# Kernel optimization log

Hardware: AMD Instinct MI355X
Metric: run time of the kernel (lower is better)

Reference implementation:

```python
import jax, jax.numpy as jnp
import numpy as np

N_NODES = 100000
N_EDGES = 1000000
KEY_DIM = 128
VAL_DIM = 64


def setup_inputs() -> dict:
    key = jax.random.key(0)
    k0, k1, k2, k3, k4, k5 = jax.random.split(key, 6)
    triples = jax.random.randint(k0, (N_EDGES, 3), 0, N_NODES, dtype=jnp.int64)
    ent_feats = jax.random.normal(k1, (N_NODES, KEY_DIM), dtype=jnp.float32)
    att_feats = jax.random.normal(k2, (N_NODES, KEY_DIM), dtype=jnp.float32)
    val_feats = jax.random.normal(k3, (N_NODES, VAL_DIM), dtype=jnp.float32)
    # a: Linear(2*key_dim, 1) -> weight vector [2k], bias [1]
    a_w = jax.random.normal(k4, (2 * KEY_DIM,), dtype=jnp.float32) * (1.0 / np.sqrt(2 * KEY_DIM))
    a_b = jnp.zeros((1,), dtype=jnp.float32)
    W = jax.random.normal(k5, (KEY_DIM + VAL_DIM, KEY_DIM), dtype=jnp.float32) * (1.0 / np.sqrt(KEY_DIM + VAL_DIM))
    return {"attribute_triples": triples, "ent_feats": ent_feats,
            "att_feats": att_feats, "val_feats": val_feats,
            "a_w": a_w, "a_b": a_b, "W": W}


def reference(attribute_triples, ent_feats, att_feats, val_feats, a_w, a_b, W):
    N = ent_feats.shape[0]
    h = attribute_triples[:, 0]
    att = attribute_triples[:, 1]
    val = attribute_triples[:, 2]
    # edge attention score: a([e_h ; a_att]) -> leaky_relu -> exp
    e_h = ent_feats[h]            # [E, K]
    a_f = att_feats[att]          # [E, K]
    score = jnp.concatenate((e_h, a_f), axis=-1) @ a_w + a_b[0]   # [E]
    score = jnp.exp(jax.nn.leaky_relu(score, negative_slope=0.2))
    # segment softmax denominator per head node
    row_sum = jax.ops.segment_sum(score, h, num_segments=N)       # [N]
    attention_p = score / row_sum[h]                               # [E]
    # projected edge messages, weighted by attention, scattered to nodes
    av = jnp.concatenate((a_f, val_feats[val]), axis=-1) @ W       # [E, K]
    av = av * attention_p[:, None]
    to_feats = jax.ops.segment_sum(av, h, num_segments=N)          # [N, K]
    return jax.nn.elu(to_feats + ent_feats)
```

## Files before the change

kernel.cpp:

```cpp
#include <hip/hip_runtime.h>

#define N_NODES 100000
#define N_EDGES 1000000
#define CAP     40

typedef __attribute__((ext_vector_type(8))) short short8;
typedef __attribute__((ext_vector_type(4))) short short4v;
typedef __attribute__((ext_vector_type(4))) float float4_t;
typedef __attribute__((ext_vector_type(2))) float floatx2;
typedef unsigned long long ull;

__device__ __forceinline__ unsigned short f_to_bf(float f) {
    union { float f; unsigned int i; } c; c.f = f;
    unsigned int x = c.i;
    unsigned int r = x + 0x7fffu + ((x >> 16) & 1u);
    return (unsigned short)(r >> 16);
}
__device__ __forceinline__ float bf_to_f(unsigned short u) {
    union { unsigned int i; float f; } c; c.i = ((unsigned int)u) << 16; return c.f;
}
__device__ __forceinline__ unsigned int pack2(float x, float y) {
    return (unsigned int)f_to_bf(x) | ((unsigned int)f_to_bf(y) << 16);
}
__device__ __forceinline__ unsigned short f_to_h(float f) {
    union { float f; unsigned int i; } c; c.f = f;
    unsigned int i = c.i;
    unsigned int e = ((i >> 23) & 0xffu) - 112u;
    unsigned int m = i & 0x7fffffu;
    unsigned int r = (e << 10) | (m >> 13);
    r += (m >> 12) & 1u;
    return (unsigned short)r;
}
__device__ __forceinline__ float h_to_f(unsigned short h) {
    union { unsigned int i; float f; } c;
    c.i = (((unsigned int)(h & 0x7fffu)) << 13) + 0x38000000u;
    return c.f;
}
__device__ __forceinline__ floatx2 up2(unsigned int u) {
    union { unsigned int i; float f; } lo, hi;
    lo.i = u << 16; hi.i = u & 0xffff0000u;
    floatx2 r; r.x = lo.f; r.y = hi.f; return r;
}
__device__ __forceinline__ int clampi(int x) {
    return x < 0 ? 0 : (x >= N_NODES ? N_NODES - 1 : x);
}

__global__ __launch_bounds__(256)
void k_node_scores(const float* __restrict__ ent,
                   const float* __restrict__ attf,
                   const float* __restrict__ valf,
                   const float* __restrict__ aw,
                   float* __restrict__ s_ent, float* __restrict__ s_att,
                   unsigned short* __restrict__ attb,
                   unsigned short* __restrict__ valb) {
    int node = (int)((blockIdx.x * blockDim.x + threadIdx.x) >> 6);
    int lane = threadIdx.x & 63;
    if (node >= N_NODES) return;
    const float2* aw2 = (const float2*)aw;
    float2 we = aw2[lane];
    float2 wa = aw2[64 + lane];
    float2 e2 = ((const float2*)ent)[(size_t)node * 64 + lane];
    float2 a2 = ((const float2*)attf)[(size_t)node * 64 + lane];
    if (attb) ((unsigned int*)attb)[(size_t)node * 64 + lane] = pack2(a2.x, a2.y);
    if (valb) valb[(size_t)node * 64 + lane] = f_to_bf(valf[(size_t)node * 64 + lane]);
    float se = e2.x * we.x + e2.y * we.y;
    float sa = a2.x * wa.x + a2.y * wa.y;
#pragma unroll
    for (int off = 32; off >= 1; off >>= 1) {
        se += __shfl_xor(se, off, 64);
        sa += __shfl_xor(sa, off, 64);
    }
    if (lane == 0) { s_ent[node] = se; s_att[node] = sa; }
}

__global__ __launch_bounds__(256)
void k_prepW(const float* __restrict__ W, unsigned short* __restrict__ Wt) {
    int i = (int)(blockIdx.x * blockDim.x + threadIdx.x);
    if (i >= 192 * 128) return;
    int c = i / 192, k = i - c * 192;
    Wt[i] = f_to_bf(W[k * 128 + c]);
}

__global__ __launch_bounds__(256)
void k_place(const int* __restrict__ tri,
             const float* __restrict__ s_ent, const float* __restrict__ s_att,
             const float* __restrict__ abp,
             int* __restrict__ cursor, ull* __restrict__ edges) {
    int e = (int)(blockIdx.x * blockDim.x + threadIdx.x);
    if (e >= N_EDGES) return;
    int h = clampi(tri[3 * e]);
    int a = clampi(tri[3 * e + 1]);
    int v = clampi(tri[3 * e + 2]);
    float s = s_ent[h] + s_att[a] + abp[0];
    s = s > 0.f ? s : 0.2f * s;
    float sc = __expf(s);
    int slot = atomicAdd(&cursor[h], 1);
    if (slot < CAP) {
        ull pk = (ull)(unsigned)a | ((ull)(unsigned)v << 17) | ((ull)f_to_h(sc) << 34);
        edges[(size_t)h * CAP + slot] = pk;
    }
}

__global__ __launch_bounds__(256)
void k_fused_bf(const int* __restrict__ cursor, const ull* __restrict__ edges,
                const unsigned short* __restrict__ attb, const unsigned short* __restrict__ valb,
                const unsigned short* __restrict__ Wt, const float* __restrict__ ent,
                float* __restrict__ out) {
    __shared__ unsigned short Gl[16][200];
    int w = threadIdx.x >> 6, lane = threadIdx.x & 63;
    int grp = lane >> 4, l = lane & 15;
    int base = (int)blockIdx.x * 16;
    int nb = base + w * 4;

    int4 cnt4 = *(const int4*)(cursor + nb);
    int li = lane < CAP ? lane : CAP - 1;
    ull edr[4];
#pragma unroll
    for (int nn = 0; nn < 4; ++nn) edr[nn] = edges[(size_t)(nb + nn) * CAP + li];

    const char* ab = (const char*)attb;
    const char* vb = (const char*)valb;

#pragma unroll
    for (int nn = 0; nn < 4; ++nn) {
        int cnt = (nn == 0) ? cnt4.x : (nn == 1) ? cnt4.y : (nn == 2) ? cnt4.z : cnt4.w;
        cnt = cnt > CAP ? CAP : cnt;
        ull edreg = edr[nn];
        floatx2 aa0 = {0.f, 0.f}, aa1 = {0.f, 0.f}, aa2 = {0.f, 0.f}, aa3 = {0.f, 0.f};
        floatx2 av0 = {0.f, 0.f}, av1 = {0.f, 0.f};
        float rsum = 0.f;
        int kmax = (cnt + 7) >> 3;
        for (int k = 0; k < kmax; ++k) {
            int j0 = grp + (k << 3), j1 = j0 + 4;
            bool m0 = j0 < cnt, m1 = j1 < cnt;
            ull e0 = __shfl(edreg, m0 ? j0 : 0, 64);
            ull e1 = __shfl(edreg, m1 ? j1 : 0, 64);
            unsigned a0 = m0 ? (unsigned)(e0 & 0x1FFFFu) : (unsigned)N_NODES;
            unsigned v0 = m0 ? (unsigned)((e0 >> 17) & 0x1FFFFu) : (unsigned)N_NODES;
            float   sc0 = m0 ? h_to_f((unsigned short)(e0 >> 34)) : 0.f;
            unsigned a1 = m1 ? (unsigned)(e1 & 0x1FFFFu) : (unsigned)N_NODES;
            unsigned v1 = m1 ? (unsigned)((e1 >> 17) & 0x1FFFFu) : (unsigned)N_NODES;
            float   sc1 = m1 ? h_to_f((unsigned short)(e1 >> 34)) : 0.f;
            uint4 A0 = *(const uint4*)(ab + (a0 << 8) + (l << 4));
            uint2 V0 = *(const uint2*)(vb + (v0 << 7) + (l << 3));
            uint4 A1 = *(const uint4*)(ab + (a1 << 8) + (l << 4));
            uint2 V1 = *(const uint2*)(vb + (v1 << 7) + (l << 3));
            rsum += sc0 + sc1;
            floatx2 s0; s0.x = sc0; s0.y = sc0;
            floatx2 s1; s1.x = sc1; s1.y = sc1;
            aa0 += s0 * up2(A0.x); aa1 += s0 * up2(A0.y);
            aa2 += s0 * up2(A0.z); aa3 += s0 * up2(A0.w);
            av0 += s0 * up2(V0.x); av1 += s0 * up2(V0.y);
            aa0 += s1 * up2(A1.x); aa1 += s1 * up2(A1.y);
            aa2 += s1 * up2(A1.z); aa3 += s1 * up2(A1.w);
            av0 += s1 * up2(V1.x); av1 += s1 * up2(V1.y);
        }
#define RED2(x) x += __shfl_xor(x, 16, 64); x += __shfl_xor(x, 32, 64)
        RED2(aa0.x); RED2(aa0.y); RED2(aa1.x); RED2(aa1.y);
        RED2(aa2.x); RED2(aa2.y); RED2(aa3.x); RED2(aa3.y);
        RED2(av0.x); RED2(av0.y); RED2(av1.x); RED2(av1.y);
        RED2(rsum);
#undef RED2
        if (grp == 0) {
            float inv = rsum > 0.f ? 1.f / rsum : 0.f;
            unsigned short* gp = &Gl[w * 4 + nn][0];
            uint4 pk;
            pk.x = pack2(aa0.x * inv, aa0.y * inv);
            pk.y = pack2(aa1.x * inv, aa1.y * inv);
            pk.z = pack2(aa2.x * inv, aa2.y * inv);
            pk.w = pack2(aa3.x * inv, aa3.y * inv);
            *(uint4*)(gp + l * 8) = pk;
            uint2 pv; pv.x = pack2(av0.x * inv, av0.y * inv);
            pv.y = pack2(av1.x * inv, av1.y * inv);
            *(uint2*)(gp + 128 + l * 4) = pv;
        }
    }
    __syncthreads();

    int quad = grp, mn = l;
    float4_t acc0 = {0.f, 0.f, 0.f, 0.f}, acc1 = {0.f, 0.f, 0.f, 0.f};
#pragma unroll
    for (int kt = 0; kt < 6; ++kt) {
        short8 afr = *(const short8*)(&Gl[mn][quad * 8 + kt * 32]);
        short8 b0 = *(const short8*)(Wt + (size_t)((w * 2 + 0) * 16 + mn) * 192 + quad * 8 + kt * 32);
        short8 b1 = *(const short8*)(Wt + (size_t)((w * 2 + 1) * 16 + mn) * 192 + quad * 8 + kt * 32);
        acc0 = __builtin_amdgcn_mfma_f32_16x16x32_bf16(afr, b0, acc0, 0, 0, 0);
        acc1 = __builtin_amdgcn_mfma_f32_16x16x32_bf16(afr, b1, acc1, 0, 0, 0);
    }
#pragma unroll
    for (int cti = 0; cti < 2; ++cti) {
        float4_t acc = cti ? acc1 : acc0;
        int col = (w * 2 + cti) * 16 + mn;
#pragma unroll
        for (int r = 0; r < 4; ++r) {
            int node = base + quad * 4 + r;
            float x = acc[r] + ent[(size_t)node * 128 + col];
            out[(size_t)node * 128 + col] = x > 0.f ? x : expm1f(x);
        }
    }
}

template<int ABF, int VBF>
__global__ __launch_bounds__(256)
void k_fused(const int* __restrict__ cursor, const ull* __restrict__ edges,
             const float* __restrict__ attf, const float* __restrict__ valf,
             const unsigned short* __restrict__ attb, const unsigned short* __restrict__ valb,
             const unsigned short* __restrict__ Wt, const float* __restrict__ ent,
             float* __restrict__ out) {
    __shared__ unsigned short Gl[16][200];
    int w = threadIdx.x >> 6, lane = threadIdx.x & 63;
    int grp = lane >> 4, l = lane & 15;
    int base = (int)blockIdx.x * 16;

    for (int nn = 0; nn < 4; ++nn) {
        int node = base + w * 4 + nn;
        int cnt = cursor[node]; if (cnt > CAP) cnt = CAP;
        size_t beg = (size_t)node * CAP;
        float aa[8] = {0.f, 0.f, 0.f, 0.f, 0.f, 0.f, 0.f, 0.f};
        float av[4] = {0.f, 0.f, 0.f, 0.f};
        float rsum = 0.f;
        for (int j = grp; j < cnt; j += 4) {
            ull ed = edges[beg + j];
            int a = (int)(ed & 0x1FFFFu);
            int v = (int)((ed >> 17) & 0x1FFFFu);
            float sc = h_to_f((unsigned short)(ed >> 34));
            rsum += sc;
            if (ABF) {
                short8 af = *(const short8*)(attb + (size_t)a * 128 + l * 8);
#pragma unroll
                for (int q = 0; q < 8; ++q) aa[q] += sc * bf_to_f((unsigned short)af[q]);
            } else {
                const float4_t* ap = (const float4_t*)(attf + (size_t)a * 128);
                float4_t f0 = ap[l], f1 = ap[16 + l];
#pragma unroll
                for (int q = 0; q < 4; ++q) { aa[q] += sc * f0[q]; aa[4 + q] += sc * f1[q]; }
            }
            if (VBF) {
                short4v vf = *(const short4v*)(valb + (size_t)v * 64 + l * 4);
#pragma unroll
                for (int q = 0; q < 4; ++q) av[q] += sc * bf_to_f((unsigned short)vf[q]);
            } else {
                float4_t fv = ((const float4_t*)(valf + (size_t)v * 64))[l];
#pragma unroll
                for (int q = 0; q < 4; ++q) av[q] += sc * fv[q];
            }
        }
#pragma unroll
        for (int q = 0; q < 8; ++q) {
            aa[q] += __shfl_xor(aa[q], 16, 64);
            aa[q] += __shfl_xor(aa[q], 32, 64);
        }
#pragma unroll
        for (int q = 0; q < 4; ++q) {
            av[q] += __shfl_xor(av[q], 16, 64);
            av[q] += __shfl_xor(av[q], 32, 64);
        }
        rsum += __shfl_xor(rsum, 16, 64);
        rsum += __shfl_xor(rsum, 32, 64);
        if (grp == 0) {
            float inv = rsum > 0.f ? 1.f / rsum : 0.f;
            unsigned short* gp = &Gl[w * 4 + nn][0];
            if (ABF) {
                uint4 pk;
                pk.x = pack2(aa[0] * inv, aa[1] * inv);
                pk.y = pack2(aa[2] * inv, aa[3] * inv);
                pk.z = pack2(aa[4] * inv, aa[5] * inv);
                pk.w = pack2(aa[6] * inv, aa[7] * inv);
                *(uint4*)(gp + l * 8) = pk;
            } else {
                uint2 p0; p0.x = pack2(aa[0] * inv, aa[1] * inv); p0.y = pack2(aa[2] * inv, aa[3] * inv);
                *(uint2*)(gp + l * 4) = p0;
                uint2 p1; p1.x = pack2(aa[4] * inv, aa[5] * inv); p1.y = pack2(aa[6] * inv, aa[7] * inv);
                *(uint2*)(gp + 64 + l * 4) = p1;
            }
            uint2 pv; pv.x = pack2(av[0] * inv, av[1] * inv); pv.y = pack2(av[2] * inv, av[3] * inv);
            *(uint2*)(gp + 128 + l * 4) = pv;
        }
    }
    __syncthreads();

    int quad = grp, mn = l;
    float4_t acc0 = {0.f, 0.f, 0.f, 0.f}, acc1 = {0.f, 0.f, 0.f, 0.f};
#pragma unroll
    for (int kt = 0; kt < 6; ++kt) {
        short8 afr = *(const short8*)(&Gl[mn][quad * 8 + kt * 32]);
        short8 b0 = *(const short8*)(Wt + (size_t)((w * 2 + 0) * 16 + mn) * 192 + quad * 8 + kt * 32);
        short8 b1 = *(const short8*)(Wt + (size_t)((w * 2 + 1) * 16 + mn) * 192 + quad * 8 + kt * 32);
        acc0 = __builtin_amdgcn_mfma_f32_16x16x32_bf16(afr, b0, acc0, 0, 0, 0);
        acc1 = __builtin_amdgcn_mfma_f32_16x16x32_bf16(afr, b1, acc1, 0, 0, 0);
    }
#pragma unroll
    for (int cti = 0; cti < 2; ++cti) {
        float4_t acc = cti ? acc1 : acc0;
        int col = (w * 2 + cti) * 16 + mn;
#pragma unroll
        for (int r = 0; r < 4; ++r) {
            int node = base + quad * 4 + r;
            float x = acc[r] + ent[(size_t)node * 128 + col];
            out[(size_t)node * 128 + col] = x > 0.f ? x : expm1f(x);
        }
    }
}

extern "C" void kernel_launch(void* const* d_in, const int* in_sizes, int n_in,
                              void* d_out, int out_size, void* d_ws, size_t ws_size,
                              hipStream_t stream) {
    const int*   tri  = (const int*)d_in[0];
    const float* ent  = (const float*)d_in[1];
    const float* attf = (const float*)d_in[2];
    const float* valf = (const float*)d_in[3];
    const float* aw   = (const float*)d_in[4];
    const float* ab   = (const float*)d_in[5];
    const float* W    = (const float*)d_in[6];
    float* out = (float*)d_out;

    char* ws = (char*)d_ws;
    size_t off = 0;
    int*   cursor = (int*)(ws + off);   off += (size_t)N_NODES * 4;
    float* s_ent  = (float*)(ws + off); off += (size_t)N_NODES * 4;
    float* s_att  = (float*)(ws + off); off += (size_t)N_NODES * 4;
    unsigned short* Wt = (unsigned short*)(ws + off); off += 192 * 128 * 2;
    ull* edges = (ull*)(ws + off);      off += (size_t)N_NODES * CAP * 8;
    unsigned short* attb = (unsigned short*)(ws + off);
    off += (size_t)(N_NODES + 1) * 128 * 2;
    size_t need_a = off;
    unsigned short* valb = (unsigned short*)(ws + off);
    off += (size_t)(N_NODES + 1) * 64 * 2;
    size_t need_av = off;
    int abf = ws_size >= need_a;
    int vbf = ws_size >= need_av;

    hipMemsetAsync(cursor, 0, (size_t)N_NODES * 4, stream);
    if (abf) hipMemsetAsync(attb + (size_t)N_NODES * 128, 0, 256, stream);
    if (vbf) hipMemsetAsync(valb + (size_t)N_NODES * 64, 0, 128, stream);

    k_node_scores<<<N_NODES / 4, 256, 0, stream>>>(ent, attf, valf, aw, s_ent, s_att,
                                                   abf ? attb : (unsigned short*)nullptr,
                                                   vbf ? valb : (unsigned short*)nullptr);
    k_prepW<<<(192 * 128 + 255) / 256, 256, 0, stream>>>(W, Wt);
    k_place<<<(N_EDGES + 255) / 256, 256, 0, stream>>>(tri, s_ent, s_att, ab, cursor, edges);
    if (abf && vbf)
        k_fused_bf<<<N_NODES / 16, 256, 0, stream>>>(cursor, edges, attb, valb, Wt, ent, out);
    else if (abf)
        k_fused<1, 0><<<N_NODES / 16, 256, 0, stream>>>(cursor, edges, attf, valf, attb, valb, Wt, ent, out);
    else
        k_fused<0, 0><<<N_NODES / 16, 256, 0, stream>>>(cursor, edges, attf, valf, attb, valb, Wt, ent, out);
}
```

Before: 332.0 us.

## Switch gathered features and weights to fp16 with packed half accumulation

Converts the attribute/value feature tables and W from bf16 to fp16, and accumulates the per-edge weighted sums with packed fp16 vector math (including the cross-lane reductions) instead of fp32. The MFMA switches to the f16 variant. Nontemporal loads and stores are added on triples, the edge list, ent and out, and masked edges now gather row 0 instead of a zeroed sentinel row. The aim is to halve accumulation ALU and register cost and to reduce cache pollution, at the risk of fp16 overflow or precision loss when summing up to 40 scaled features.

```diff
diff --git a/kernel.cpp b/kernel.cpp
--- a/kernel.cpp
+++ b/kernel.cpp
@@ -4,24 +4,14 @@
 #define N_EDGES 1000000
 #define CAP     40
 
-typedef __attribute__((ext_vector_type(8))) short short8;
-typedef __attribute__((ext_vector_type(4))) short short4v;
 typedef __attribute__((ext_vector_type(4))) float float4_t;
-typedef __attribute__((ext_vector_type(2))) float floatx2;
+typedef __attribute__((ext_vector_type(2))) _Float16 half2v;
+typedef __attribute__((ext_vector_type(4))) _Float16 half4v;
+typedef __attribute__((ext_vector_type(8))) _Float16 half8v;
+typedef __attribute__((ext_vector_type(2))) unsigned int uint2v;
+typedef __attribute__((ext_vector_type(4))) unsigned int uint4v;
 typedef unsigned long long ull;
 
-__device__ __forceinline__ unsigned short f_to_bf(float f) {
-    union { float f; unsigned int i; } c; c.f = f;
-    unsigned int x = c.i;
-    unsigned int r = x + 0x7fffu + ((x >> 16) & 1u);
-    return (unsigned short)(r >> 16);
-}
-__device__ __forceinline__ float bf_to_f(unsigned short u) {
-    union { unsigned int i; float f; } c; c.i = ((unsigned int)u) << 16; return c.f;
-}
-__device__ __forceinline__ unsigned int pack2(float x, float y) {
-    return (unsigned int)f_to_bf(x) | ((unsigned int)f_to_bf(y) << 16);
-}
 __device__ __forceinline__ unsigned short f_to_h(float f) {
     union { float f; unsigned int i; } c; c.f = f;
     unsigned int i = c.i;
@@ -36,10 +26,15 @@
     c.i = (((unsigned int)(h & 0x7fffu)) << 13) + 0x38000000u;
     return c.f;
 }
-__device__ __forceinline__ floatx2 up2(unsigned int u) {
-    union { unsigned int i; float f; } lo, hi;
-    lo.i = u << 16; hi.i = u & 0xffff0000u;
-    floatx2 r; r.x = lo.f; r.y = hi.f; return r;
+__device__ __forceinline__ unsigned int packh2(float x, float y) {
+    half2v h; h.x = (_Float16)x; h.y = (_Float16)y;
+    return __builtin_bit_cast(unsigned int, h);
+}
+__device__ __forceinline__ unsigned int h2add(unsigned int a, unsigned int b) {
+    half2v x = __builtin_bit_cast(half2v, a);
+    half2v y = __builtin_bit_cast(half2v, b);
+    half2v r = x + y;
+    return __builtin_bit_cast(unsigned int, r);
 }
 __device__ __forceinline__ int clampi(int x) {
     return x < 0 ? 0 : (x >= N_NODES ? N_NODES - 1 : x);
@@ -61,8 +56,11 @@
     float2 wa = aw2[64 + lane];
     float2 e2 = ((const float2*)ent)[(size_t)node * 64 + lane];
     float2 a2 = ((const float2*)attf)[(size_t)node * 64 + lane];
-    if (attb) ((unsigned int*)attb)[(size_t)node * 64 + lane] = pack2(a2.x, a2.y);
-    if (valb) valb[(size_t)node * 64 + lane] = f_to_bf(valf[(size_t)node * 64 + lane]);
+    if (attb) ((unsigned int*)attb)[(size_t)node * 64 + lane] = packh2(a2.x, a2.y);
+    if (valb) {
+        float vv = valf[(size_t)node * 64 + lane];
+        valb[(size_t)node * 64 + lane] = __builtin_bit_cast(unsigned short, (_Float16)vv);
+    }
     float se = e2.x * we.x + e2.y * we.y;
     float sa = a2.x * wa.x + a2.y * wa.y;
 #pragma unroll
@@ -78,7 +76,7 @@
     int i = (int)(blockIdx.x * blockDim.x + threadIdx.x);
     if (i >= 192 * 128) return;
     int c = i / 192, k = i - c * 192;
-    Wt[i] = f_to_bf(W[k * 128 + c]);
+    Wt[i] = __builtin_bit_cast(unsigned short, (_Float16)W[k * 128 + c]);
 }
 
 __global__ __launch_bounds__(256)
@@ -88,24 +86,24 @@
              int* __restrict__ cursor, ull* __restrict__ edges) {
     int e = (int)(blockIdx.x * blockDim.x + threadIdx.x);
     if (e >= N_EDGES) return;
-    int h = clampi(tri[3 * e]);
-    int a = clampi(tri[3 * e + 1]);
-    int v = clampi(tri[3 * e + 2]);
+    int h = clampi(__builtin_nontemporal_load(tri + 3 * e));
+    int a = clampi(__builtin_nontemporal_load(tri + 3 * e + 1));
+    int v = clampi(__builtin_nontemporal_load(tri + 3 * e + 2));
     float s = s_ent[h] + s_att[a] + abp[0];
     s = s > 0.f ? s : 0.2f * s;
     float sc = __expf(s);
     int slot = atomicAdd(&cursor[h], 1);
     if (slot < CAP) {
         ull pk = (ull)(unsigned)a | ((ull)(unsigned)v << 17) | ((ull)f_to_h(sc) << 34);
-        edges[(size_t)h * CAP + slot] = pk;
-    }
-}
-
-__global__ __launch_bounds__(256)
-void k_fused_bf(const int* __restrict__ cursor, const ull* __restrict__ edges,
-                const unsigned short* __restrict__ attb, const unsigned short* __restrict__ valb,
-                const unsigned short* __restrict__ Wt, const float* __restrict__ ent,
-                float* __restrict__ out) {
+        __builtin_nontemporal_store(pk, edges + (size_t)h * CAP + slot);
+    }
+}
+
+__global__ __launch_bounds__(256)
+void k_fused_h(const int* __restrict__ cursor, const ull* __restrict__ edges,
+               const unsigned short* __restrict__ attb, const unsigned short* __restrict__ valb,
+               const unsigned short* __restrict__ Wt, const float* __restrict__ ent,
+               float* __restrict__ out) {
     __shared__ unsigned short Gl[16][200];
     int w = threadIdx.x >> 6, lane = threadIdx.x & 63;
     int grp = lane >> 4, l = lane & 15;
@@ -113,21 +111,23 @@
     int nb = base + w * 4;
 
     int4 cnt4 = *(const int4*)(cursor + nb);
-    int li = lane < CAP ? lane : CAP - 1;
+    int cns[4] = {cnt4.x, cnt4.y, cnt4.z, cnt4.w};
     ull edr[4];
 #pragma unroll
-    for (int nn = 0; nn < 4; ++nn) edr[nn] = edges[(size_t)(nb + nn) * CAP + li];
-
-    const char* ab = (const char*)attb;
-    const char* vb = (const char*)valb;
-
-#pragma unroll
     for (int nn = 0; nn < 4; ++nn) {
-        int cnt = (nn == 0) ? cnt4.x : (nn == 1) ? cnt4.y : (nn == 2) ? cnt4.z : cnt4.w;
-        cnt = cnt > CAP ? CAP : cnt;
+        int c = cns[nn]; c = c > CAP ? CAP : c; cns[nn] = c;
+        int li = lane < c ? lane : 0;
+        edr[nn] = __builtin_nontemporal_load(edges + (size_t)(nb + nn) * CAP + li);
+    }
+    const half8v* ap = (const half8v*)attb;
+    const half4v* vp = (const half4v*)valb;
+
+#pragma unroll
+    for (int nn = 0; nn < 4; ++nn) {
+        int cnt = cns[nn];
         ull edreg = edr[nn];
-        floatx2 aa0 = {0.f, 0.f}, aa1 = {0.f, 0.f}, aa2 = {0.f, 0.f}, aa3 = {0.f, 0.f};
-        floatx2 av0 = {0.f, 0.f}, av1 = {0.f, 0.f};
+        half8v accA = {};
+        half4v accV = {};
         float rsum = 0.f;
         int kmax = (cnt + 7) >> 3;
         for (int k = 0; k < kmax; ++k) {
@@ -135,44 +135,46 @@
             bool m0 = j0 < cnt, m1 = j1 < cnt;
             ull e0 = __shfl(edreg, m0 ? j0 : 0, 64);
             ull e1 = __shfl(edreg, m1 ? j1 : 0, 64);
-            unsigned a0 = m0 ? (unsigned)(e0 & 0x1FFFFu) : (unsigned)N_NODES;
-            unsigned v0 = m0 ? (unsigned)((e0 >> 17) & 0x1FFFFu) : (unsigned)N_NODES;
-            float   sc0 = m0 ? h_to_f((unsigned short)(e0 >> 34)) : 0.f;
-            unsigned a1 = m1 ? (unsigned)(e1 & 0x1FFFFu) : (unsigned)N_NODES;
-            unsigned v1 = m1 ? (unsigned)((e1 >> 17) & 0x1FFFFu) : (unsigned)N_NODES;
-            float   sc1 = m1 ? h_to_f((unsigned short)(e1 >> 34)) : 0.f;
-            uint4 A0 = *(const uint4*)(ab + (a0 << 8) + (l << 4));
-            uint2 V0 = *(const uint2*)(vb + (v0 << 7) + (l << 3));
-            uint4 A1 = *(const uint4*)(ab + (a1 << 8) + (l << 4));
-            uint2 V1 = *(const uint2*)(vb + (v1 << 7) + (l << 3));
-            rsum += sc0 + sc1;
-            floatx2 s0; s0.x = sc0; s0.y = sc0;
-            floatx2 s1; s1.x = sc1; s1.y = sc1;
-            aa0 += s0 * up2(A0.x); aa1 += s0 * up2(A0.y);
-            aa2 += s0 * up2(A0.z); aa3 += s0 * up2(A0.w);
-            av0 += s0 * up2(V0.x); av1 += s0 * up2(V0.y);
-            aa0 += s1 * up2(A1.x); aa1 += s1 * up2(A1.y);
-            aa2 += s1 * up2(A1.z); aa3 += s1 * up2(A1.w);
-            av0 += s1 * up2(V1.x); av1 += s1 * up2(V1.y);
-        }
-#define RED2(x) x += __shfl_xor(x, 16, 64); x += __shfl_xor(x, 32, 64)
-        RED2(aa0.x); RED2(aa0.y); RED2(aa1.x); RED2(aa1.y);
-        RED2(aa2.x); RED2(aa2.y); RED2(aa3.x); RED2(aa3.y);
-        RED2(av0.x); RED2(av0.y); RED2(av1.x); RED2(av1.y);
-        RED2(rsum);
-#undef RED2
+            int a0 = (int)(e0 & 0x1FFFFu), v0 = (int)((e0 >> 17) & 0x1FFFFu);
+            int a1 = (int)(e1 & 0x1FFFFu), v1 = (int)((e1 >> 17) & 0x1FFFFu);
+            _Float16 s0 = m0 ? __builtin_bit_cast(_Float16, (unsigned short)(e0 >> 34)) : (_Float16)0.f;
+            _Float16 s1 = m1 ? __builtin_bit_cast(_Float16, (unsigned short)(e1 >> 34)) : (_Float16)0.f;
+            half8v A0 = ap[a0 * 16 + l];
+            half4v V0 = vp[v0 * 16 + l];
+            half8v A1 = ap[a1 * 16 + l];
+            half4v V1 = vp[v1 * 16 + l];
+            rsum += (float)s0 + (float)s1;
+            accA += A0 * s0;
+            accV += V0 * s0;
+            accA += A1 * s1;
+            accV += V1 * s1;
+        }
+        uint4v ua = __builtin_bit_cast(uint4v, accA);
+        uint2v uv = __builtin_bit_cast(uint2v, accV);
+#pragma unroll
+        for (int q = 0; q < 4; ++q) {
+            unsigned int x = ua[q];
+            x = h2add(x, __shfl_xor(x, 16, 64));
+            x = h2add(x, __shfl_xor(x, 32, 64));
+            ua[q] = x;
+        }
+#pragma unroll
+        for (int q = 0; q < 2; ++q) {
+            unsigned int x = uv[q];
+            x = h2add(x, __shfl_xor(x, 16, 64));
+            x = h2add(x, __shfl_xor(x, 32, 64));
+            uv[q] = x;
+        }
+        rsum += __shfl_xor(rsum, 16, 64);
+        rsum += __shfl_xor(rsum, 32, 64);
         if (grp == 0) {
             float inv = rsum > 0.f ? 1.f / rsum : 0.f;
+            _Float16 ih = (_Float16)inv;
+            half8v gA = __builtin_bit_cast(half8v, ua) * ih;
+            half4v gV = __builtin_bit_cast(half4v, uv) * ih;
             unsigned short* gp = &Gl[w * 4 + nn][0];
-            uint4 pk;
-            pk.x = pack2(aa0.x * inv, aa0.y * inv);
-            pk.y = pack2(aa1.x * inv, aa1.y * inv);
-            pk.z = pack2(aa2.x * inv, aa2.y * inv);
-            pk.w = pack2(aa3.x * inv, aa3.y * inv);
-            *(uint4*)(gp + l * 8) = pk;
-            uint2 pv; pv.x = pack2(av0.x * inv, av0.y * inv);
-            pv.y = pack2(av1.x * inv, av1.y * inv);
-            *(uint2*)(gp + 128 + l * 4) = pv;
+            *(half8v*)(gp + l * 8) = gA;
+            *(half4v*)(gp + 128 + l * 4) = gV;
         }
     }
     __syncthreads();
@@ -181,11 +183,11 @@
     float4_t acc0 = {0.f, 0.f, 0.f, 0.f}, acc1 = {0.f, 0.f, 0.f, 0.f};
 #pragma unroll
     for (int kt = 0; kt < 6; ++kt) {
-        short8 afr = *(const short8*)(&Gl[mn][quad * 8 + kt * 32]);
-        short8 b0 = *(const short8*)(Wt + (size_t)((w * 2 + 0) * 16 + mn) * 192 + quad * 8 + kt * 32);
-        short8 b1 = *(const short8*)(Wt + (size_t)((w * 2 + 1) * 16 + mn) * 192 + quad * 8 + kt * 32);
-        acc0 = __builtin_amdgcn_mfma_f32_16x16x32_bf16(afr, b0, acc0, 0, 0, 0);
-        acc1 = __builtin_amdgcn_mfma_f32_16x16x32_bf16(afr, b1, acc1, 0, 0, 0);
+        half8v afr = *(const half8v*)(&Gl[mn][quad * 8 + kt * 32]);
+        half8v b0 = *(const half8v*)(Wt + (size_t)((w * 2 + 0) * 16 + mn) * 192 + quad * 8 + kt * 32);
+        half8v b1 = *(const half8v*)(Wt + (size_t)((w * 2 + 1) * 16 + mn) * 192 + quad * 8 + kt * 32);
+        acc0 = __builtin_amdgcn_mfma_f32_16x16x32_f16(afr, b0, acc0, 0, 0, 0);
+        acc1 = __builtin_amdgcn_mfma_f32_16x16x32_f16(afr, b1, acc1, 0, 0, 0);
     }
 #pragma unroll
     for (int cti = 0; cti < 2; ++cti) {
@@ -194,19 +196,18 @@
 #pragma unroll
         for (int r = 0; r < 4; ++r) {
             int node = base + quad * 4 + r;
-            float x = acc[r] + ent[(size_t)node * 128 + col];
-            out[(size_t)node * 128 + col] = x > 0.f ? x : expm1f(x);
-        }
-    }
-}
-
-template<int ABF, int VBF>
-__global__ __launch_bounds__(256)
-void k_fused(const int* __restrict__ cursor, const ull* __restrict__ edges,
-             const float* __restrict__ attf, const float* __restrict__ valf,
-             const unsigned short* __restrict__ attb, const unsigned short* __restrict__ valb,
-             const unsigned short* __restrict__ Wt, const float* __restrict__ ent,
-             float* __restrict__ out) {
+            float x = acc[r] + __builtin_nontemporal_load(ent + (size_t)node * 128 + col);
+            __builtin_nontemporal_store(x > 0.f ? x : expm1f(x),
+                                        out + (size_t)node * 128 + col);
+        }
+    }
+}
+
+__global__ __launch_bounds__(256)
+void k_fused_f32(const int* __restrict__ cursor, const ull* __restrict__ edges,
+                 const float* __restrict__ attf, const float* __restrict__ valf,
+                 const unsigned short* __restrict__ Wt, const float* __restrict__ ent,
+                 float* __restrict__ out) {
     __shared__ unsigned short Gl[16][200];
     int w = threadIdx.x >> 6, lane = threadIdx.x & 63;
     int grp = lane >> 4, l = lane & 15;
@@ -225,24 +226,12 @@
             int v = (int)((ed >> 17) & 0x1FFFFu);
             float sc = h_to_f((unsigned short)(ed >> 34));
             rsum += sc;
-            if (ABF) {
-                short8 af = *(const short8*)(attb + (size_t)a * 128 + l * 8);
-#pragma unroll
-                for (int q = 0; q < 8; ++q) aa[q] += sc * bf_to_f((unsigned short)af[q]);
-            } else {
-                const float4_t* ap = (const float4_t*)(attf + (size_t)a * 128);
-                float4_t f0 = ap[l], f1 = ap[16 + l];
-#pragma unroll
-                for (int q = 0; q < 4; ++q) { aa[q] += sc * f0[q]; aa[4 + q] += sc * f1[q]; }
-            }
-            if (VBF) {
-                short4v vf = *(const short4v*)(valb + (size_t)v * 64 + l * 4);
-#pragma unroll
-                for (int q = 0; q < 4; ++q) av[q] += sc * bf_to_f((unsigned short)vf[q]);
-            } else {
-                float4_t fv = ((const float4_t*)(valf + (size_t)v * 64))[l];
-#pragma unroll
-                for (int q = 0; q < 4; ++q) av[q] += sc * fv[q];
+            const float4_t* ap = (const float4_t*)(attf + (size_t)a * 128);
+            float4_t f0 = ap[l], f1 = ap[16 + l];
+            float4_t fv = ((const float4_t*)(valf + (size_t)v * 64))[l];
+#pragma unroll
+            for (int q = 0; q < 4; ++q) {
+                aa[q] += sc * f0[q]; aa[4 + q] += sc * f1[q]; av[q] += sc * fv[q];
             }
         }
 #pragma unroll
@@ -260,20 +249,11 @@
         if (grp == 0) {
             float inv = rsum > 0.f ? 1.f / rsum : 0.f;
             unsigned short* gp = &Gl[w * 4 + nn][0];
-            if (ABF) {
-                uint4 pk;
-                pk.x = pack2(aa[0] * inv, aa[1] * inv);
-                pk.y = pack2(aa[2] * inv, aa[3] * inv);
-                pk.z = pack2(aa[4] * inv, aa[5] * inv);
-                pk.w = pack2(aa[6] * inv, aa[7] * inv);
-                *(uint4*)(gp + l * 8) = pk;
-            } else {
-                uint2 p0; p0.x = pack2(aa[0] * inv, aa[1] * inv); p0.y = pack2(aa[2] * inv, aa[3] * inv);
-                *(uint2*)(gp + l * 4) = p0;
-                uint2 p1; p1.x = pack2(aa[4] * inv, aa[5] * inv); p1.y = pack2(aa[6] * inv, aa[7] * inv);
-                *(uint2*)(gp + 64 + l * 4) = p1;
-            }
-            uint2 pv; pv.x = pack2(av[0] * inv, av[1] * inv); pv.y = pack2(av[2] * inv, av[3] * inv);
+            uint2 p0; p0.x = packh2(aa[0] * inv, aa[1] * inv); p0.y = packh2(aa[2] * inv, aa[3] * inv);
+            *(uint2*)(gp + l * 4) = p0;
+            uint2 p1; p1.x = packh2(aa[4] * inv, aa[5] * inv); p1.y = packh2(aa[6] * inv, aa[7] * inv);
+            *(uint2*)(gp + 64 + l * 4) = p1;
+            uint2 pv; pv.x = packh2(av[0] * inv, av[1] * inv); pv.y = packh2(av[2] * inv, av[3] * inv);
             *(uint2*)(gp + 128 + l * 4) = pv;
         }
     }
@@ -283,11 +263,11 @@
     float4_t acc0 = {0.f, 0.f, 0.f, 0.f}, acc1 = {0.f, 0.f, 0.f, 0.f};
 #pragma unroll
     for (int kt = 0; kt < 6; ++kt) {
-        short8 afr = *(const short8*)(&Gl[mn][quad * 8 + kt * 32]);
-        short8 b0 = *(const short8*)(Wt + (size_t)((w * 2 + 0) * 16 + mn) * 192 + quad * 8 + kt * 32);
-        short8 b1 = *(const short8*)(Wt + (size_t)((w * 2 + 1) * 16 + mn) * 192 + quad * 8 + kt * 32);
-        acc0 = __builtin_amdgcn_mfma_f32_16x16x32_bf16(afr, b0, acc0, 0, 0, 0);
-        acc1 = __builtin_amdgcn_mfma_f32_16x16x32_bf16(afr, b1, acc1, 0, 0, 0);
+        half8v afr = *(const half8v*)(&Gl[mn][quad * 8 + kt * 32]);
+        half8v b0 = *(const half8v*)(Wt + (size_t)((w * 2 + 0) * 16 + mn) * 192 + quad * 8 + kt * 32);
+        half8v b1 = *(const half8v*)(Wt + (size_t)((w * 2 + 1) * 16 + mn) * 192 + quad * 8 + kt * 32);
+        acc0 = __builtin_amdgcn_mfma_f32_16x16x32_f16(afr, b0, acc0, 0, 0, 0);
+        acc1 = __builtin_amdgcn_mfma_f32_16x16x32_f16(afr, b1, acc1, 0, 0, 0);
     }
 #pragma unroll
     for (int cti = 0; cti < 2; ++cti) {
@@ -321,28 +301,20 @@
     float* s_att  = (float*)(ws + off); off += (size_t)N_NODES * 4;
     unsigned short* Wt = (unsigned short*)(ws + off); off += 192 * 128 * 2;
     ull* edges = (ull*)(ws + off);      off += (size_t)N_NODES * CAP * 8;
-    unsigned short* attb = (unsigned short*)(ws + off);
-    off += (size_t)(N_NODES + 1) * 128 * 2;
-    size_t need_a = off;
-    unsigned short* valb = (unsigned short*)(ws + off);
-    off += (size_t)(N_NODES + 1) * 64 * 2;
-    size_t need_av = off;
-    int abf = ws_size >= need_a;
-    int vbf = ws_size >= need_av;
+    unsigned short* attb = (unsigned short*)(ws + off); off += (size_t)N_NODES * 128 * 2;
+    unsigned short* valb = (unsigned short*)(ws + off); off += (size_t)N_NODES * 64 * 2;
+    size_t need = off;
+    int h16 = ws_size >= need;
 
     hipMemsetAsync(cursor, 0, (size_t)N_NODES * 4, stream);
-    if (abf) hipMemsetAsync(attb + (size_t)N_NODES * 128, 0, 256, stream);
-    if (vbf) hipMemsetAsync(valb + (size_t)N_NODES * 64, 0, 128, stream);
 
     k_node_scores<<<N_NODES / 4, 256, 0, stream>>>(ent, attf, valf, aw, s_ent, s_att,
-                                                   abf ? attb : (unsigned short*)nullptr,
-                                                   vbf ? valb : (unsigned short*)nullptr);
+                                                   h16 ? attb : (unsigned short*)nullptr,
+                                                   h16 ? valb : (unsigned short*)nullptr);
     k_prepW<<<(192 * 128 + 255) / 256, 256, 0, stream>>>(W, Wt);
     k_place<<<(N_EDGES + 255) / 256, 256, 0, stream>>>(tri, s_ent, s_att, ab, cursor, edges);
-    if (abf && vbf)
-        k_fused_bf<<<N_NODES / 16, 256, 0, stream>>>(cursor, edges, attb, valb, Wt, ent, out);
-    else if (abf)
-        k_fused<1, 0><<<N_NODES / 16, 256, 0, stream>>>(cursor, edges, attf, valf, attb, valb, Wt, ent, out);
+    if (h16)
+        k_fused_h<<<N_NODES / 16, 256, 0, stream>>>(cursor, edges, attb, valb, Wt, ent, out);
     else
-        k_fused<0, 0><<<N_NODES / 16, 256, 0, stream>>>(cursor, edges, attf, valf, attb, valb, Wt, ent, out);
-}
+        k_fused_f32<<<N_NODES / 16, 256, 0, stream>>>(cursor, edges, attf, valf, Wt, ent, out);
+}
```

Result: no change. 334.4 us (+0.7%).
